# Performance work log

Measured on AMD Instinct MI355X. Metric: run time of the kernel, lower is better.

The kernel has to match this reference:

```python
import jax, jax.numpy as jnp
import numpy as np

BS, NQ, NK = 4096, 21, 7   # batch, num_neg queries, 7 keys (weekdays)
E = 512                     # key_size == query_size
H = 512                     # hidden_size
NEG_INF = -1e9


def setup_inputs() -> dict:
    key = jax.random.key(0)
    ks = jax.random.split(key, 6)
    sq = 1.0 / np.sqrt(E)
    sh = 1.0 / np.sqrt(H)
    return {
        "queries": jax.random.normal(ks[0], (BS, NQ, E), jnp.float32),
        "keys": jax.random.normal(ks[1], (BS, NK, E), jnp.float32),
        "wq_w": jax.random.normal(ks[2], (H, E), jnp.float32) * sq,
        "wq_b": jnp.zeros((H,), jnp.float32),
        "wk_w": jax.random.normal(ks[3], (H, E), jnp.float32) * sq,
        "wk_b": jnp.zeros((H,), jnp.float32),
        "wv_w": jax.random.normal(ks[4], (1, H), jnp.float32) * sh,
        "wv_b": jnp.zeros((1,), jnp.float32),
        "cum_subs_masks": jax.random.randint(ks[5], (BS, 1, NK, 1), 0, 2).astype(jnp.int32),
        "num_neg": NQ,
    }


def reference(queries, keys, wq_w, wq_b, wk_w, wk_b, wv_w, wv_b, cum_subs_masks, num_neg):
    # dropout p=0.0 -> identity (as in eval / p=0)
    q = jnp.einsum('bqe,he->bqh', queries, wq_w) + wq_b          # (bs,21,H)
    k = jnp.einsum('bke,he->bkh', keys, wk_w) + wk_b             # (bs,7,H)
    # additive score: broadcast q over keys, k over queries
    t = jnp.tanh(q[:, :, None, :] + k[:, None, :, :])            # (bs,21,7,H)
    scores = jnp.einsum('bqkh,oh->bqko', t, wv_w) + wv_b         # (bs,21,7,1)
    scores = scores + cum_subs_masks.astype(scores.dtype) * NEG_INF
    attn_weights = jax.nn.softmax(scores, axis=-2)               # softmax over 7 keys
    # weighted sum of the RAW keys (the module multiplies by expanded `keys`)
    attn_out = jnp.einsum('bqk,bke->bqe', attn_weights[..., 0], keys)  # (bs,21,E)
    return (attn_out, attn_weights)
```

## Files before the change

### kernel.cpp

```cpp
#include <hip/hip_runtime.h>
#include <hip/hip_bf16.h>

#define BS_   4096
#define NQ_   21
#define NK_   7
#define E_    512
#define MQ_   (BS_*NQ_)
#define MK_   (BS_*NK_)
#define MTQ_  (MQ_/64)
#define MTK_  (MK_/64)
#define MTT_  (MTQ_+MTK_)
#define SCALE_ 2.88539008177792681f

typedef __attribute__((ext_vector_type(8))) short bf16x8;
typedef __attribute__((ext_vector_type(4))) float f32x4;
typedef __attribute__((ext_vector_type(8))) unsigned short u16x8;

__device__ __forceinline__ unsigned int cvt_pk_bf16(float lo, float hi){
  unsigned int r;
  asm("v_cvt_pk_bf16_f32 %0, %1, %2" : "=v"(r) : "v"(lo), "v"(hi));
  return r;
}
__device__ __forceinline__ float bf2f(unsigned short h){
  return __builtin_bit_cast(float, (unsigned int)h << 16);
}

__global__ __launch_bounds__(256) void cast_weights(
    const float* __restrict__ wq, const float* __restrict__ wk,
    unsigned int* __restrict__ oq, unsigned int* __restrict__ ok)
{
  int i = blockIdx.x * 256 + threadIdx.x;
  float4 a = ((const float4*)wq)[i];
  float4 b = ((const float4*)wk)[i];
  uint2 ua = { cvt_pk_bf16(a.x, a.y), cvt_pk_bf16(a.z, a.w) };
  uint2 ub = { cvt_pk_bf16(b.x, b.y), cvt_pk_bf16(b.z, b.w) };
  ((uint2*)oq)[i] = ua;
  ((uint2*)ok)[i] = ub;
}

__global__ __launch_bounds__(256)
void gemm_proj(const float* __restrict__ Aq, const float* __restrict__ Ak,
               const unsigned short* __restrict__ Bq, const unsigned short* __restrict__ Bk,
               const float* __restrict__ bq, const float* __restrict__ bk,
               unsigned short* __restrict__ Cq, unsigned short* __restrict__ Ck)
{
  __shared__ char Asm[2][64 * 64];

  const int tid  = threadIdx.x;
  const int lane = tid & 63;
  const int w    = tid >> 6;

  const int bid = (int)blockIdx.x;
  const int j   = bid >> 3;
  int       mt  = (j >> 1) * 8 + (bid & 7);
  const int ntb = j & 1;

  const float* A; const unsigned short* Bw; const float* bias; unsigned short* C;
  if (mt < MTQ_){ A = Aq; Bw = Bq; bias = bq; C = Cq; }
  else          { A = Ak; Bw = Bk; bias = bk; C = Ck; mt -= MTQ_; }

  const long m0  = (long)mt << 6;
  const int  n0w = ntb * 256 + w * 64;
  const char* Abyte = (const char*)(A + m0 * E_);

  long asrc[2]; int adst[2];
#pragma unroll
  for (int i = 0; i < 2; ++i){
    const int c   = tid + i * 256;
    const int row = c >> 3;
    const int sl  = c & 7;
    asrc[i] = (long)row * (E_ * 4) + sl * 16;
    adst[i] = row * 64 + (((sl & 6) * 8) ^ (((row >> 1) & 3) << 4)) + (sl & 1) * 8;
  }
  int aoff[4];
#pragma unroll
  for (int m = 0; m < 4; ++m){
    const int r = m * 16 + (lane & 15);
    aoff[m] = r * 64 + ((16 * (lane >> 4)) ^ (((r >> 1) & 3) << 4));
  }
  const unsigned short* Bp = Bw + (long)(n0w + (lane & 15)) * E_ + (lane >> 4) * 8;

  f32x4 acc[4][4];
  const f32x4 z4 = {0.f, 0.f, 0.f, 0.f};
#pragma unroll
  for (int m = 0; m < 4; ++m)
#pragma unroll
    for (int n = 0; n < 4; ++n) acc[m][n] = z4;

  bf16x8 bfrC[4], bfrN[4];
  float4 avA[2], avB[2];

#define LOAD_A(av, T) do { \
  _Pragma("unroll") for (int i_ = 0; i_ < 2; ++i_) \
    av[i_] = *(const float4*)(Abyte + asrc[i_] + (long)(T) * 128); \
} while(0)

#define LOAD_B(dst, T) do { \
  _Pragma("unroll") for (int n_ = 0; n_ < 4; ++n_) \
    dst[n_] = *(const bf16x8*)(Bp + (long)n_ * 16 * E_ + (T) * 32); \
} while(0)

#define WRITE_A(BUF, av) do { \
  _Pragma("unroll") for (int i_ = 0; i_ < 2; ++i_){ \
    uint2 u_ = { cvt_pk_bf16(av[i_].x, av[i_].y), cvt_pk_bf16(av[i_].z, av[i_].w) }; \
    *(uint2*)(Asm[BUF] + adst[i_]) = u_; \
  } \
} while(0)

#define COMPUTE(BUF) do { \
  bf16x8 af_[4]; \
  _Pragma("unroll") for (int m_ = 0; m_ < 4; ++m_) \
    af_[m_] = *(const bf16x8*)(Asm[BUF] + aoff[m_]); \
  _Pragma("unroll") for (int m_ = 0; m_ < 4; ++m_) \
    _Pragma("unroll") for (int n_ = 0; n_ < 4; ++n_) \
      acc[m_][n_] = __builtin_amdgcn_mfma_f32_16x16x32_bf16(af_[m_], bfrC[n_], acc[m_][n_], 0, 0, 0); \
} while(0)

#define BAR() do { \
  asm volatile("s_waitcnt lgkmcnt(0)" ::: "memory"); \
  __builtin_amdgcn_s_barrier(); \
  __builtin_amdgcn_sched_barrier(0); \
} while(0)

#define STEP(T, AVISS, AVWR) do { \
  LOAD_A(AVISS, (T) + 2); \
  LOAD_B(bfrN, (T) + 1); \
  COMPUTE((T) & 1); \
  WRITE_A(((T) + 1) & 1, AVWR); \
  BAR(); \
  _Pragma("unroll") for (int n_ = 0; n_ < 4; ++n_) bfrC[n_] = bfrN[n_]; \
} while(0)

  LOAD_A(avA, 0);
  LOAD_A(avB, 1);
  LOAD_B(bfrC, 0);
  WRITE_A(0, avA);
  BAR();

#pragma unroll
  for (int tp = 0; tp < 7; ++tp){
    const int t = tp * 2;
    STEP(t,     avA, avB);
    STEP(t + 1, avB, avA);
  }
  {
    LOAD_B(bfrN, 15);
    COMPUTE(0);
    WRITE_A(1, avB);
    BAR();
#pragma unroll
    for (int n_ = 0; n_ < 4; ++n_) bfrC[n_] = bfrN[n_];
  }
  COMPUTE(1);

#undef LOAD_A
#undef LOAD_B
#undef WRITE_A
#undef COMPUTE
#undef BAR
#undef STEP

  const int ccol0 = n0w + (lane & 15);
  float bvs[4];
#pragma unroll
  for (int n = 0; n < 4; ++n) bvs[n] = bias[ccol0 + n * 16] * SCALE_;
#pragma unroll
  for (int m = 0; m < 4; ++m){
    const long rbase = m0 + m * 16 + (lane >> 4) * 4;
#pragma unroll
    for (int n = 0; n < 4; ++n){
      const long col = ccol0 + n * 16;
      float v0 = fmaf(acc[m][n][0], SCALE_, bvs[n]);
      float v1 = fmaf(acc[m][n][1], SCALE_, bvs[n]);
      float v2 = fmaf(acc[m][n][2], SCALE_, bvs[n]);
      float v3 = fmaf(acc[m][n][3], SCALE_, bvs[n]);
      unsigned int u01 = cvt_pk_bf16(v0, v1);
      unsigned int u23 = cvt_pk_bf16(v2, v3);
      C[(rbase + 0) * E_ + col] = (unsigned short)(u01 & 0xffffu);
      C[(rbase + 1) * E_ + col] = (unsigned short)(u01 >> 16);
      C[(rbase + 2) * E_ + col] = (unsigned short)(u23 & 0xffffu);
      C[(rbase + 3) * E_ + col] = (unsigned short)(u23 >> 16);
    }
  }
}

__global__ __launch_bounds__(256, 2)
void attn_fused(const unsigned short* __restrict__ qp,
                const unsigned short* __restrict__ kp,
                const float* __restrict__ keys,
                const float* __restrict__ wv, const float* __restrict__ wvb,
                const int* __restrict__ mask,
                float* __restrict__ out0, float* __restrict__ out1)
{
  const int lane = threadIdx.x & 63;
  const int b    = blockIdx.x * 4 + (threadIdx.x >> 6);

  float wvr[8];
  *(float4*)&wvr[0] = ((const float4*)wv)[lane * 2];
  *(float4*)&wvr[4] = ((const float4*)wv)[lane * 2 + 1];

  float kf[NK_][8];
#pragma unroll
  for (int k = 0; k < NK_; ++k){
    u16x8 u = *(const u16x8*)(kp + ((long)b * NK_ + k) * E_ + lane * 8);
#pragma unroll
    for (int j = 0; j < 8; ++j) kf[k][j] = bf2f((unsigned short)u[j]);
  }
  float kr[NK_][8];
#pragma unroll
  for (int k = 0; k < NK_; ++k){
    const float4* p = (const float4*)(keys + ((long)b * NK_ + k) * E_ + lane * 8);
    *(float4*)&kr[k][0] = p[0];
    *(float4*)&kr[k][4] = p[1];
  }

  float wsum = ((wvr[0] + wvr[1]) + (wvr[2] + wvr[3])) + ((wvr[4] + wvr[5]) + (wvr[6] + wvr[7]));
#pragma unroll
  for (int off = 32; off; off >>= 1) wsum += __shfl_xor(wsum, off, 64);

  const float vb = wvb[0];
  float base[NK_];
#pragma unroll
  for (int k = 0; k < NK_; ++k)
    base[k] = (wsum + vb) + (float)mask[b * NK_ + k] * (-1e9f);

  const unsigned short* qrow = qp + (long)b * NQ_ * E_ + lane * 8;
  u16x8 qv = *(const u16x8*)qrow;

  float4* o0 = (float4*)(out0 + (long)b * NQ_ * E_) + lane * 2;
  float*  o1 = out1 + (long)b * (NQ_ * NK_);

  for (int qi = 0; qi < NQ_; ++qi){
    u16x8 qn = qv;
    if (qi < NQ_ - 1) qn = *(const u16x8*)(qrow + (qi + 1) * E_);

    float qf[8];
#pragma unroll
    for (int j = 0; j < 8; ++j) qf[j] = bf2f((unsigned short)qv[j]);
    qv = qn;

    float acc[NK_];
#pragma unroll
    for (int k = 0; k < NK_; ++k){
      float a = 0.f;
#pragma unroll
      for (int j = 0; j < 8; ++j){
        float x = qf[j] + kf[k][j];
        float e = __builtin_amdgcn_exp2f(x);
        float r = __builtin_amdgcn_rcpf(e + 1.0f);
        a = fmaf(wvr[j], r, a);
      }
      acc[k] = a;
    }
#pragma unroll
    for (int k = 0; k < NK_; ++k){
      float a = acc[k];
#pragma unroll
      for (int off = 32; off; off >>= 1) a += __shfl_xor(a, off, 64);
      acc[k] = a;
    }
    float sc[NK_], mx = -3.4e38f;
#pragma unroll
    for (int k = 0; k < NK_; ++k){ sc[k] = fmaf(-2.f, acc[k], base[k]); mx = fmaxf(mx, sc[k]); }
    float sum = 0.f;
#pragma unroll
    for (int k = 0; k < NK_; ++k){ sc[k] = __expf(sc[k] - mx); sum += sc[k]; }
    const float inv = __builtin_amdgcn_rcpf(sum);
    float wgt[NK_];
#pragma unroll
    for (int k = 0; k < NK_; ++k) wgt[k] = sc[k] * inv;

    float wsel = wgt[0];
#pragma unroll
    for (int k = 1; k < NK_; ++k) wsel = (lane == k) ? wgt[k] : wsel;
    if (lane < NK_) o1[qi * NK_ + lane] = wsel;

    float4 lo = {0.f,0.f,0.f,0.f}, hi = {0.f,0.f,0.f,0.f};
#pragma unroll
    for (int k = 0; k < NK_; ++k){
      lo.x = fmaf(wgt[k], kr[k][0], lo.x);
      lo.y = fmaf(wgt[k], kr[k][1], lo.y);
      lo.z = fmaf(wgt[k], kr[k][2], lo.z);
      lo.w = fmaf(wgt[k], kr[k][3], lo.w);
      hi.x = fmaf(wgt[k], kr[k][4], hi.x);
      hi.y = fmaf(wgt[k], kr[k][5], hi.y);
      hi.z = fmaf(wgt[k], kr[k][6], hi.z);
      hi.w = fmaf(wgt[k], kr[k][7], hi.w);
    }
    o0[qi * 128 + 0] = lo;
    o0[qi * 128 + 1] = hi;
  }
}

extern "C" void kernel_launch(void* const* d_in, const int* in_sizes, int n_in,
                              void* d_out, int out_size, void* d_ws, size_t ws_size,
                              hipStream_t stream)
{
  const float* queries = (const float*)d_in[0];
  const float* keys    = (const float*)d_in[1];
  const float* wq_w    = (const float*)d_in[2];
  const float* wq_b    = (const float*)d_in[3];
  const float* wk_w    = (const float*)d_in[4];
  const float* wk_b    = (const float*)d_in[5];
  const float* wv_w    = (const float*)d_in[6];
  const float* wv_b    = (const float*)d_in[7];
  const int*   mask    = (const int*)d_in[8];
  (void)in_sizes; (void)n_in; (void)out_size; (void)ws_size;

  float* out0 = (float*)d_out;
  float* out1 = out0 + (long)MQ_ * E_;

  char* ws = (char*)d_ws;
  unsigned short* wqb = (unsigned short*)ws;
  unsigned short* wkb = (unsigned short*)(ws + 512 * 512 * 2);
  unsigned short* qb  = (unsigned short*)(ws + (1 << 20));
  unsigned short* kb  = qb + (size_t)MQ_ * E_;

  cast_weights<<<dim3(256), dim3(256), 0, stream>>>(wq_w, wk_w, (unsigned int*)wqb, (unsigned int*)wkb);
  gemm_proj<<<dim3(MTT_ * 2), dim3(256), 0, stream>>>(
      queries, keys, wqb, wkb, wq_b, wk_b, qb, kb);
  attn_fused<<<dim3(BS_ / 4), dim3(256), 0, stream>>>(qb, kb, keys, wv_w, wv_b, mask, out0, out1);
}
```

Before: 293.4 us.

## Stage full 64x512 A tile in LDS and compute all 512 columns per block

The projection GEMM now has each block own a 64-row M tile across the full N=512, instead of splitting N into two 256-wide blocks. The whole bf16-converted A tile (64 KB) is loaded into shared memory once with an XOR swizzle, so the fp32 activations are read from global memory once instead of twice. The K loop then runs without barriers, double-buffering only the B fragments from global. Block order is remapped across XCD-style groups. The cost is 64 KB of LDS and a 4x8 accumulator set per wave, which lowers occupancy, and no A loads overlap with MFMA work.

```diff
diff --git a/kernel.cpp b/kernel.cpp
--- a/kernel.cpp
+++ b/kernel.cpp
@@ -8,8 +8,7 @@
 #define MQ_   (BS_*NQ_)
 #define MK_   (BS_*NK_)
 #define MTQ_  (MQ_/64)
-#define MTK_  (MK_/64)
-#define MTT_  (MTQ_+MTK_)
+#define MTT_  ((MQ_+MK_)/64)
 #define SCALE_ 2.88539008177792681f
 
 typedef __attribute__((ext_vector_type(8))) short bf16x8;
@@ -44,131 +43,113 @@
                const float* __restrict__ bq, const float* __restrict__ bk,
                unsigned short* __restrict__ Cq, unsigned short* __restrict__ Ck)
 {
-  __shared__ char Asm[2][64 * 64];
+  __shared__ char Asm[64 * 1024];
 
   const int tid  = threadIdx.x;
   const int lane = tid & 63;
   const int w    = tid >> 6;
-
-  const int bid = (int)blockIdx.x;
-  const int j   = bid >> 3;
-  int       mt  = (j >> 1) * 8 + (bid & 7);
-  const int ntb = j & 1;
+  const int l15  = lane & 15;
+  const int s4   = lane >> 4;
+
+  const int orig = (int)blockIdx.x;
+  int mt = (orig & 7) * (MTT_ / 8) + (orig >> 3);
 
   const float* A; const unsigned short* Bw; const float* bias; unsigned short* C;
   if (mt < MTQ_){ A = Aq; Bw = Bq; bias = bq; C = Cq; }
   else          { A = Ak; Bw = Bk; bias = bk; C = Ck; mt -= MTQ_; }
 
   const long m0  = (long)mt << 6;
-  const int  n0w = ntb * 256 + w * 64;
+  const int  n0w = w << 7;
   const char* Abyte = (const char*)(A + m0 * E_);
 
-  long asrc[2]; int adst[2];
-#pragma unroll
-  for (int i = 0; i < 2; ++i){
-    const int c   = tid + i * 256;
-    const int row = c >> 3;
-    const int sl  = c & 7;
-    asrc[i] = (long)row * (E_ * 4) + sl * 16;
-    adst[i] = row * 64 + (((sl & 6) * 8) ^ (((row >> 1) & 3) << 4)) + (sl & 1) * 8;
-  }
-  int aoff[4];
+  const unsigned short* Bpn[8];
+#pragma unroll
+  for (int n = 0; n < 8; ++n)
+    Bpn[n] = Bw + (long)(n0w + n * 16 + l15) * E_ + s4 * 8;
+
+  int aoffE[4], aoffO[4];
 #pragma unroll
   for (int m = 0; m < 4; ++m){
-    const int r = m * 16 + (lane & 15);
-    aoff[m] = r * 64 + ((16 * (lane >> 4)) ^ (((r >> 1) & 3) << 4));
-  }
-  const unsigned short* Bp = Bw + (long)(n0w + (lane & 15)) * E_ + (lane >> 4) * 8;
-
-  f32x4 acc[4][4];
+    const int r  = m * 16 + l15;
+    const int b2 = (r >> 2) & 1;
+    const int bs = r * 1024 + ((s4 ^ (r & 3)) << 4);
+    aoffE[m] = bs + b2 * 64;
+    aoffO[m] = bs - b2 * 64;
+  }
+
+  f32x4 acc[4][8];
   const f32x4 z4 = {0.f, 0.f, 0.f, 0.f};
 #pragma unroll
   for (int m = 0; m < 4; ++m)
 #pragma unroll
-    for (int n = 0; n < 4; ++n) acc[m][n] = z4;
-
-  bf16x8 bfrC[4], bfrN[4];
-  float4 avA[2], avB[2];
-
-#define LOAD_A(av, T) do { \
-  _Pragma("unroll") for (int i_ = 0; i_ < 2; ++i_) \
-    av[i_] = *(const float4*)(Abyte + asrc[i_] + (long)(T) * 128); \
-} while(0)
-
-#define LOAD_B(dst, T) do { \
-  _Pragma("unroll") for (int n_ = 0; n_ < 4; ++n_) \
-    dst[n_] = *(const bf16x8*)(Bp + (long)n_ * 16 * E_ + (T) * 32); \
-} while(0)
-
-#define WRITE_A(BUF, av) do { \
-  _Pragma("unroll") for (int i_ = 0; i_ < 2; ++i_){ \
-    uint2 u_ = { cvt_pk_bf16(av[i_].x, av[i_].y), cvt_pk_bf16(av[i_].z, av[i_].w) }; \
-    *(uint2*)(Asm[BUF] + adst[i_]) = u_; \
+    for (int n = 0; n < 8; ++n) acc[m][n] = z4;
+
+  bf16x8 b0[8], b1[8];
+
+#pragma unroll
+  for (int n = 0; n < 8; ++n)
+    b0[n] = *(const bf16x8*)((const char*)Bpn[n]);
+
+#define AISSUE(buf, g) do { \
+  _Pragma("unroll") for (int ii = 0; ii < 8; ++ii){ \
+    const int c_ = tid + ((g) * 8 + ii) * 256; \
+    buf[ii] = *(const float4*)(Abyte + (long)(c_ >> 7) * 2048 + (c_ & 127) * 16); \
   } \
 } while(0)
-
-#define COMPUTE(BUF) do { \
+#define AWRITE(buf, g) do { \
+  _Pragma("unroll") for (int ii = 0; ii < 8; ++ii){ \
+    const int c_ = tid + ((g) * 8 + ii) * 256; \
+    const int row_ = c_ >> 7, sl_ = c_ & 127; \
+    uint2 u_ = { cvt_pk_bf16(buf[ii].x, buf[ii].y), cvt_pk_bf16(buf[ii].z, buf[ii].w) }; \
+    *(uint2*)(Asm + row_ * 1024 + (((sl_ >> 1) ^ (row_ & 7)) << 4) + (sl_ & 1) * 8) = u_; \
+  } \
+} while(0)
+
+  {
+    float4 avX[8], avY[8];
+    AISSUE(avX, 0);
+    AISSUE(avY, 1);
+    AWRITE(avX, 0);
+    AISSUE(avX, 2);
+    AWRITE(avY, 1);
+    AISSUE(avY, 3);
+    AWRITE(avX, 2);
+    AWRITE(avY, 3);
+  }
+  __syncthreads();
+
+#define KSTEP(T, BCUR, BNXT) do { \
+  if ((T) < 15){ \
+    _Pragma("unroll") for (int n_ = 0; n_ < 8; ++n_) \
+      BNXT[n_] = *(const bf16x8*)((const char*)Bpn[n_] + ((T) + 1) * 64); \
+  } \
   bf16x8 af_[4]; \
   _Pragma("unroll") for (int m_ = 0; m_ < 4; ++m_) \
-    af_[m_] = *(const bf16x8*)(Asm[BUF] + aoff[m_]); \
+    af_[m_] = *(const bf16x8*)(Asm + (((T) & 1) ? aoffO[m_] : aoffE[m_]) + (T) * 64); \
   _Pragma("unroll") for (int m_ = 0; m_ < 4; ++m_) \
-    _Pragma("unroll") for (int n_ = 0; n_ < 4; ++n_) \
-      acc[m_][n_] = __builtin_amdgcn_mfma_f32_16x16x32_bf16(af_[m_], bfrC[n_], acc[m_][n_], 0, 0, 0); \
+    _Pragma("unroll") for (int n_ = 0; n_ < 8; ++n_) \
+      acc[m_][n_] = __builtin_amdgcn_mfma_f32_16x16x32_bf16(af_[m_], BCUR[n_], acc[m_][n_], 0, 0, 0); \
 } while(0)
 
-#define BAR() do { \
-  asm volatile("s_waitcnt lgkmcnt(0)" ::: "memory"); \
-  __builtin_amdgcn_s_barrier(); \
-  __builtin_amdgcn_sched_barrier(0); \
-} while(0)
-
-#define STEP(T, AVISS, AVWR) do { \
-  LOAD_A(AVISS, (T) + 2); \
-  LOAD_B(bfrN, (T) + 1); \
-  COMPUTE((T) & 1); \
-  WRITE_A(((T) + 1) & 1, AVWR); \
-  BAR(); \
-  _Pragma("unroll") for (int n_ = 0; n_ < 4; ++n_) bfrC[n_] = bfrN[n_]; \
-} while(0)
-
-  LOAD_A(avA, 0);
-  LOAD_A(avB, 1);
-  LOAD_B(bfrC, 0);
-  WRITE_A(0, avA);
-  BAR();
-
-#pragma unroll
-  for (int tp = 0; tp < 7; ++tp){
-    const int t = tp * 2;
-    STEP(t,     avA, avB);
-    STEP(t + 1, avB, avA);
-  }
-  {
-    LOAD_B(bfrN, 15);
-    COMPUTE(0);
-    WRITE_A(1, avB);
-    BAR();
-#pragma unroll
-    for (int n_ = 0; n_ < 4; ++n_) bfrC[n_] = bfrN[n_];
-  }
-  COMPUTE(1);
-
-#undef LOAD_A
-#undef LOAD_B
-#undef WRITE_A
-#undef COMPUTE
-#undef BAR
-#undef STEP
-
-  const int ccol0 = n0w + (lane & 15);
-  float bvs[4];
-#pragma unroll
-  for (int n = 0; n < 4; ++n) bvs[n] = bias[ccol0 + n * 16] * SCALE_;
+#pragma unroll
+  for (int tp = 0; tp < 8; ++tp){
+    KSTEP(2 * tp,     b0, b1);
+    KSTEP(2 * tp + 1, b1, b0);
+  }
+
+#undef AISSUE
+#undef AWRITE
+#undef KSTEP
+
+  const int ccol0 = n0w + l15;
+  float bvs[8];
+#pragma unroll
+  for (int n = 0; n < 8; ++n) bvs[n] = bias[ccol0 + n * 16] * SCALE_;
 #pragma unroll
   for (int m = 0; m < 4; ++m){
-    const long rbase = m0 + m * 16 + (lane >> 4) * 4;
-#pragma unroll
-    for (int n = 0; n < 4; ++n){
+    const long rbase = m0 + m * 16 + s4 * 4;
+#pragma unroll
+    for (int n = 0; n < 8; ++n){
       const long col = ccol0 + n * 16;
       float v0 = fmaf(acc[m][n][0], SCALE_, bvs[n]);
       float v1 = fmaf(acc[m][n][1], SCALE_, bvs[n]);
@@ -317,7 +298,7 @@
   unsigned short* kb  = qb + (size_t)MQ_ * E_;
 
   cast_weights<<<dim3(256), dim3(256), 0, stream>>>(wq_w, wk_w, (unsigned int*)wqb, (unsigned int*)wkb);
-  gemm_proj<<<dim3(MTT_ * 2), dim3(256), 0, stream>>>(
+  gemm_proj<<<dim3(MTT_), dim3(256), 0, stream>>>(
       queries, keys, wqb, wkb, wq_b, wk_b, qb, kb);
   attn_fused<<<dim3(BS_ / 4), dim3(256), 0, stream>>>(qb, kb, keys, wv_w, wv_b, mask, out0, out1);
 }
```

After: 289.9 us. About the same (-1.2%).
